# Performance work log

Hardware: AMD Instinct MI355X
Metric: run time of the kernel (lower is better)

The kernel has to match this reference:

```python
import jax, jax.numpy as jnp
import numpy as np

NUM_HEADS = 4
GROUPS = 32
EPS = 1e-5


def group_norm(x, gamma, beta):
    B, C, H, W = x.shape
    xg = x.reshape(B, GROUPS, C // GROUPS, H, W)
    mu = xg.mean(axis=(2, 3, 4), keepdims=True)
    var = xg.var(axis=(2, 3, 4), keepdims=True)
    xg = (xg - mu) * jax.lax.rsqrt(var + EPS)
    return xg.reshape(B, C, H, W) * gamma[None, :, None, None] + beta[None, :, None, None]


def setup_inputs() -> dict:
    key = jax.random.key(0)
    ks = jax.random.split(key, 6)
    B, C, H, W = 16, 256, 32, 32
    x = jax.random.normal(ks[0], (B, C, H, W), dtype=jnp.float32)
    gn_gamma = jnp.ones((C,), dtype=jnp.float32)
    gn_beta = jnp.zeros((C,), dtype=jnp.float32)
    # 1x1 convs are pure channel GEMMs; store weights as [out_ch, in_ch]
    qkv_w = jax.random.normal(ks[1], (3 * C, C), dtype=jnp.float32) * (C ** -0.5)
    qkv_b = jnp.zeros((3 * C,), dtype=jnp.float32)
    # NOTE: original zero-inits proj; we use small random weights so the
    # attention path is exercised/testable (see notes).
    proj_w = jax.random.normal(ks[2], (C, C), dtype=jnp.float32) * 0.02
    proj_b = jnp.zeros((C,), dtype=jnp.float32)
    return {"x": x, "gn_gamma": gn_gamma, "gn_beta": gn_beta,
            "qkv_w": qkv_w, "qkv_b": qkv_b, "proj_w": proj_w, "proj_b": proj_b}


def reference(x, gn_gamma, gn_beta, qkv_w, qkv_b, proj_w, proj_b):
    B, C, H, W = x.shape
    N = H * W
    d = C // NUM_HEADS
    h = group_norm(x, gn_gamma, gn_beta)
    hf = h.reshape(B, C, N)  # [B, C, N]
    qkv = jnp.einsum('oc,bcn->bon', qkv_w, hf) + qkv_b[None, :, None]
    qkv = qkv.reshape(B, NUM_HEADS, 3 * d, N)
    q, k, v = jnp.split(qkv, 3, axis=2)  # each [B, h, d, N]
    scale = d ** -0.5
    attn = jax.nn.softmax(jnp.einsum('bhdn,bhdm->bhnm', q, k) * scale, axis=-1)
    out = jnp.einsum('bhnm,bhdm->bhdn', attn, v).reshape(B, C, N)
    out = jnp.einsum('oc,bcn->bon', proj_w, out) + proj_b[None, :, None]
    return x + out.reshape(B, C, H, W)
```

## Files before the change

### kernel.cpp

```cpp
#include <hip/hip_runtime.h>

typedef short bf16x8_t __attribute__((ext_vector_type(8)));
typedef float f32x4_t __attribute__((ext_vector_type(4)));

__device__ __forceinline__ float bf2f(unsigned short h) {
  union { unsigned int u; float f; } v; v.u = ((unsigned int)h) << 16; return v.f;
}
__device__ __forceinline__ unsigned short f2bf(float f) {
  union { float f; unsigned int u; } v; v.f = f;
  unsigned int u = v.u + 0x7FFFu + ((v.u >> 16) & 1u);
  return (unsigned short)(u >> 16);
}
__device__ __forceinline__ unsigned int fbits(float f) {
  return __builtin_bit_cast(unsigned int, f);
}
__device__ __forceinline__ float exp2_hw(float x) {
  return __builtin_amdgcn_exp2f(x);
}
__device__ __forceinline__ unsigned int pack_trunc(float lo, float hi) {
  return __builtin_amdgcn_perm(fbits(hi), fbits(lo), 0x07060302u);
}
__device__ __forceinline__ void gload_lds16(const void* gsrc, void* ldst) {
  __builtin_amdgcn_global_load_lds(
      (const __attribute__((address_space(1))) unsigned int*)gsrc,
      (__attribute__((address_space(3))) unsigned int*)ldst, 16, 0, 0);
}

__device__ __align__(16) unsigned short g_hT[16 * 1024 * 256];
__device__ __align__(16) unsigned short g_qT[16 * 4 * 1024 * 64];
__device__ __align__(16) unsigned short g_kT[16 * 4 * 1024 * 64];
__device__ __align__(16) unsigned short g_vN[16 * 4 * 64 * 1024];
__device__ __align__(16) unsigned short g_wq[768 * 256];
__device__ __align__(16) unsigned short g_wp[256 * 256];

__global__ __launch_bounds__(256) void gn_kernel(
    const float* __restrict__ x, const float* __restrict__ gamma,
    const float* __restrict__ beta, const float* __restrict__ qkv_w,
    const float* __restrict__ proj_w) {
  const int b = blockIdx.x >> 5, g = blockIdx.x & 31;
  const int t = threadIdx.x;
  const float4* xg = (const float4*)(x + (size_t)(b * 256 + g * 8) * 1024);

  __shared__ __align__(16) unsigned short lds[8192];
  __shared__ float red[16];

  float vals[32];
  float s = 0.f, sq = 0.f;
#pragma unroll
  for (int p = 0; p < 4; ++p) {
    int idx = t + p * 256;
    float4 a = xg[2 * idx], c = xg[2 * idx + 1];
    float tmp[8] = {a.x, a.y, a.z, a.w, c.x, c.y, c.z, c.w};
#pragma unroll
    for (int j = 0; j < 8; ++j) {
      vals[p * 8 + j] = tmp[j];
      s += tmp[j]; sq += tmp[j] * tmp[j];
    }
  }

  {
    int widx = (blockIdx.x * 256 + t) * 2;
    const float* wsrc;
    unsigned short* wdst;
    if (widx < 196608) { wsrc = qkv_w + widx; wdst = g_wq + widx; }
    else { wsrc = proj_w + (widx - 196608); wdst = g_wp + (widx - 196608); }
    float2 wv = *(const float2*)wsrc;
    wdst[0] = f2bf(wv.x); wdst[1] = f2bf(wv.y);
  }

#pragma unroll
  for (int m = 32; m; m >>= 1) {
    s += __shfl_xor(s, m, 64);
    sq += __shfl_xor(sq, m, 64);
  }
  const int w = t >> 6;
  if ((t & 63) == 0) { red[w] = s; red[8 + w] = sq; }
  __syncthreads();
  s = red[0] + red[1] + red[2] + red[3];
  sq = red[8] + red[9] + red[10] + red[11];
  const float mu = s * (1.f / 8192.f);
  const float var = sq * (1.f / 8192.f) - mu * mu;
  const float rstd = rsqrtf(var + 1e-5f);

#pragma unroll
  for (int p = 0; p < 4; ++p) {
    int idx = t + p * 256;
    int c = idx >> 7;
    float ga = gamma[g * 8 + c] * rstd;
    float be = beta[g * 8 + c] - mu * ga;
    union { unsigned short u[8]; uint4 v; } pk;
#pragma unroll
    for (int j = 0; j < 8; ++j) pk.u[j] = f2bf(vals[p * 8 + j] * ga + be);
    ((uint4*)lds)[idx] = pk.v;
  }
  __syncthreads();

  unsigned short* dstbase = g_hT + (size_t)b * 1024 * 256 + g * 8;
#pragma unroll
  for (int p = 0; p < 4; ++p) {
    int n = t + p * 256;
    union { unsigned short u[8]; uint4 v; } pk;
#pragma unroll
    for (int c = 0; c < 8; ++c) pk.u[c] = lds[c * 1024 + n];
    *(uint4*)(dstbase + (size_t)n * 256) = pk.v;
  }
}

template <int MODE>
__global__ __launch_bounds__(256, 2) void gemm_ct(
    const float* __restrict__ bias, const float* __restrict__ xres,
    float* __restrict__ outp) {
  constexpr int OT = (MODE == 0) ? 96 : 64;
  constexpr int NT = (MODE == 0) ? 256 : 128;
  constexpr int OI = OT / 16;
  constexpr int NJ = NT / 64;
  constexpr int ASL = OT * 8;
  constexpr int BSL = NT * 8;

  const int n0 = blockIdx.x * NT;
  const int oty = blockIdx.y, o0 = oty * OT;
  const int b = blockIdx.z;
  const int t = threadIdx.x;
  const int w = t >> 6, lane = t & 63, quad = lane >> 4, l15 = lane & 15;

  __shared__ uint4 as[ASL];
  __shared__ uint4 bs[BSL];

  const uint4* Bv = (const uint4*)g_hT;
  const unsigned short* Wb = (MODE == 0) ? g_wq : g_wp;

  f32x4_t acc[OI][NJ];
#pragma unroll
  for (int i = 0; i < OI; ++i)
#pragma unroll
    for (int j = 0; j < NJ; ++j) acc[i][j] = (f32x4_t){0.f, 0.f, 0.f, 0.f};

  for (int kb = 0; kb < 4; ++kb) {
#pragma unroll
    for (int p = 0; p < ASL / 256; ++p) {
      int L = p * 256 + t;
      int row = L >> 3, kc = (L & 7) ^ (row & 7);
      gload_lds16(Wb + (size_t)(o0 + row) * 256 + kb * 64 + kc * 8,
                  &as[p * 256 + w * 64]);
    }
#pragma unroll
    for (int p = 0; p < BSL / 256; ++p) {
      int L = p * 256 + t;
      int row = L >> 3, kc = (L & 7) ^ (row & 7);
      gload_lds16(&Bv[(size_t)(b * 1024 + n0 + row) * 32 + kb * 8 + kc],
                  &bs[p * 256 + w * 64]);
    }
    __syncthreads();
#pragma unroll
    for (int kk = 0; kk < 2; ++kk) {
      int ch = kk * 4 + quad;
      const int sw = ch ^ (l15 & 7);
      bf16x8_t af[OI];
#pragma unroll
      for (int i = 0; i < OI; ++i)
        af[i] = __builtin_bit_cast(bf16x8_t, as[(i * 16 + l15) * 8 + sw]);
#pragma unroll
      for (int j = 0; j < NJ; ++j) {
        bf16x8_t bf = __builtin_bit_cast(
            bf16x8_t, bs[(w * (NT / 4) + j * 16 + l15) * 8 + sw]);
#pragma unroll
        for (int i = 0; i < OI; ++i)
          acc[i][j] = __builtin_amdgcn_mfma_f32_16x16x32_bf16(af[i], bf, acc[i][j], 0, 0, 0);
      }
    }
    __syncthreads();
  }

  float bi[OI][4];
#pragma unroll
  for (int i = 0; i < OI; ++i)
#pragma unroll
    for (int r = 0; r < 4; ++r) bi[i][r] = bias[o0 + i * 16 + quad * 4 + r];

  if (MODE == 0) {
#pragma unroll
    for (int i = 0; i < OI; ++i) {
      const int r0 = o0 + i * 16;
      const int head = r0 / 192;
      const int win = r0 - head * 192;
      const int type = win >> 6;
      const int d0 = (win & 63) + quad * 4;
      if (type < 2) {
        const float sc = (type == 0) ? 0.18033688f : 1.0f;
        unsigned short* dst = (type == 0 ? g_qT : g_kT) + (size_t)(b * 4 + head) * 65536;
#pragma unroll
        for (int j = 0; j < NJ; ++j) {
          int n = n0 + w * 64 + j * 16 + l15;
          ushort4 pk;
          pk.x = f2bf((acc[i][j][0] + bi[i][0]) * sc);
          pk.y = f2bf((acc[i][j][1] + bi[i][1]) * sc);
          pk.z = f2bf((acc[i][j][2] + bi[i][2]) * sc);
          pk.w = f2bf((acc[i][j][3] + bi[i][3]) * sc);
          *(ushort4*)(dst + (size_t)n * 64 + d0) = pk;
        }
      } else {
        unsigned short* dst = g_vN + (size_t)(b * 4 + head) * 65536;
#pragma unroll
        for (int j = 0; j < NJ; ++j) {
          int n = n0 + w * 64 + j * 16 + l15;
#pragma unroll
          for (int r = 0; r < 4; ++r)
            dst[(size_t)(d0 + r) * 1024 + n] = f2bf(acc[i][j][r] + bi[i][r]);
        }
      }
    }
  } else {
#pragma unroll
    for (int i = 0; i < OI; ++i)
#pragma unroll
      for (int r = 0; r < 4; ++r) {
        int c = o0 + i * 16 + quad * 4 + r;
        const float* xr = xres + (((size_t)b * 256 + c) << 10);
        float* op = outp + (((size_t)b * 256 + c) << 10);
#pragma unroll
        for (int j = 0; j < NJ; ++j) {
          int n = n0 + w * 32 + j * 16 + l15;
          op[n] = acc[i][j][r] + bi[i][r] + xr[n];
        }
      }
  }
}

__global__ __launch_bounds__(256) void attn_kernel() {
  const int bh = blockIdx.x;
  const int n0 = blockIdx.y * 128;
  const int t = threadIdx.x;
  const int w = t >> 6, lane = t & 63, quad = lane >> 4, l15 = lane & 15;
  const int b = bh >> 2, h = bh & 3;

  const uint4* qv = (const uint4*)(g_qT + (size_t)bh * 65536);
  const uint4* kv = (const uint4*)(g_kT + (size_t)bh * 65536);
  const uint4* vv = (const uint4*)(g_vN + (size_t)bh * 65536);

  __shared__ uint4 ks[2][512];
  __shared__ uint4 vs[2][512];
  __shared__ __align__(16) unsigned short Pt[2 * 4 * 16 * 72];

  uint4 qrA[2], qrB[2];
#pragma unroll
  for (int kk = 0; kk < 2; ++kk) {
    qrA[kk] = qv[(size_t)(n0 + w * 16 + l15) * 8 + kk * 4 + quad];
    qrB[kk] = qv[(size_t)(n0 + 64 + w * 16 + l15) * 8 + kk * 4 + quad];
  }

  const int rr0 = t >> 3, cc = t & 7, rr1 = rr0 + 32;
  uint4 kr0 = kv[rr0 * 8 + cc], kr1 = kv[rr1 * 8 + cc];
  uint4 vr0 = vv[rr0 * 128 + cc], vr1 = vv[rr1 * 128 + cc];

  f32x4_t OA[4], OB[4];
#pragma unroll
  for (int i = 0; i < 4; ++i) {
    OA[i] = (f32x4_t){0.f, 0.f, 0.f, 0.f};
    OB[i] = (f32x4_t){0.f, 0.f, 0.f, 0.f};
  }
  float rsumA = 0.f, rsumB = 0.f;

  unsigned short* PwA = Pt + w * 1152;
  unsigned short* PwB = Pt + 4608 + w * 1152;

#pragma unroll 1
  for (int mt = 0; mt < 16; ++mt) {
    uint4* kb = ks[mt & 1];
    uint4* vb = vs[mt & 1];
    kb[cc * 64 + (rr0 ^ cc)] = kr0; kb[cc * 64 + (rr1 ^ cc)] = kr1;
    vb[cc * 64 + (rr0 ^ cc)] = vr0; vb[cc * 64 + (rr1 ^ cc)] = vr1;
    __syncthreads();

    if (mt < 15) {
      int m1 = (mt + 1) * 64;
      kr0 = kv[(m1 + rr0) * 8 + cc]; kr1 = kv[(m1 + rr1) * 8 + cc];
      vr0 = vv[rr0 * 128 + (mt + 1) * 8 + cc]; vr1 = vv[rr1 * 128 + (mt + 1) * 8 + cc];
    }

    f32x4_t sA[4], sB[4];
#pragma unroll
    for (int i = 0; i < 4; ++i) {
      sA[i] = (f32x4_t){0.f, 0.f, 0.f, 0.f};
      sB[i] = (f32x4_t){0.f, 0.f, 0.f, 0.f};
    }
#pragma unroll
    for (int kk = 0; kk < 2; ++kk) {
      int ch = kk * 4 + quad;
      bf16x8_t bqA = __builtin_bit_cast(bf16x8_t, qrA[kk]);
      bf16x8_t bqB = __builtin_bit_cast(bf16x8_t, qrB[kk]);
#pragma unroll
      for (int ms = 0; ms < 4; ++ms) {
        bf16x8_t ak = __builtin_bit_cast(bf16x8_t, kb[ch * 64 + ((ms * 16 + l15) ^ ch)]);
        sA[ms] = __builtin_amdgcn_mfma_f32_16x16x32_bf16(ak, bqA, sA[ms], 0, 0, 0);
        sB[ms] = __builtin_amdgcn_mfma_f32_16x16x32_bf16(ak, bqB, sB[ms], 0, 0, 0);
      }
    }

#pragma unroll
    for (int ms = 0; ms < 4; ++ms) {
      float a0 = exp2_hw(sA[ms][0]), a1 = exp2_hw(sA[ms][1]);
      float a2 = exp2_hw(sA[ms][2]), a3 = exp2_hw(sA[ms][3]);
      float b0 = exp2_hw(sB[ms][0]), b1 = exp2_hw(sB[ms][1]);
      float b2 = exp2_hw(sB[ms][2]), b3 = exp2_hw(sB[ms][3]);
      rsumA += (a0 + a1) + (a2 + a3);
      rsumB += (b0 + b1) + (b2 + b3);
      uint2 pA, pB;
      pA.x = pack_trunc(a0, a1);
      pA.y = pack_trunc(a2, a3);
      pB.x = pack_trunc(b0, b1);
      pB.y = pack_trunc(b2, b3);
      *(uint2*)(PwA + l15 * 72 + ms * 16 + quad * 4) = pA;
      *(uint2*)(PwB + l15 * 72 + ms * 16 + quad * 4) = pB;
    }

#pragma unroll
    for (int km = 0; km < 2; ++km) {
      int ch = km * 4 + quad;
      bf16x8_t bpA = *(const bf16x8_t*)(PwA + l15 * 72 + km * 32 + quad * 8);
      bf16x8_t bpB = *(const bf16x8_t*)(PwB + l15 * 72 + km * 32 + quad * 8);
#pragma unroll
      for (int ds = 0; ds < 4; ++ds) {
        bf16x8_t av = __builtin_bit_cast(bf16x8_t, vb[ch * 64 + ((ds * 16 + l15) ^ ch)]);
        OA[ds] = __builtin_amdgcn_mfma_f32_16x16x32_bf16(av, bpA, OA[ds], 0, 0, 0);
        OB[ds] = __builtin_amdgcn_mfma_f32_16x16x32_bf16(av, bpB, OB[ds], 0, 0, 0);
      }
    }
  }

  rsumA += __shfl_xor(rsumA, 16, 64);
  rsumA += __shfl_xor(rsumA, 32, 64);
  rsumB += __shfl_xor(rsumB, 16, 64);
  rsumB += __shfl_xor(rsumB, 32, 64);
  const float invA = 1.f / rsumA, invB = 1.f / rsumB;

  unsigned short* dstA = g_hT + ((size_t)b * 1024 + n0 + w * 16 + l15) * 256 + h * 64;
  unsigned short* dstB = dstA + (size_t)64 * 256;
#pragma unroll
  for (int ds = 0; ds < 4; ++ds) {
    ushort4 pkA, pkB;
    pkA.x = f2bf(OA[ds][0] * invA); pkA.y = f2bf(OA[ds][1] * invA);
    pkA.z = f2bf(OA[ds][2] * invA); pkA.w = f2bf(OA[ds][3] * invA);
    pkB.x = f2bf(OB[ds][0] * invB); pkB.y = f2bf(OB[ds][1] * invB);
    pkB.z = f2bf(OB[ds][2] * invB); pkB.w = f2bf(OB[ds][3] * invB);
    *(ushort4*)(dstA + ds * 16 + quad * 4) = pkA;
    *(ushort4*)(dstB + ds * 16 + quad * 4) = pkB;
  }
}

extern "C" void kernel_launch(void* const* d_in, const int* in_sizes, int n_in,
                              void* d_out, int out_size, void* d_ws, size_t ws_size,
                              hipStream_t stream) {
  const float* x = (const float*)d_in[0];
  const float* gam = (const float*)d_in[1];
  const float* bet = (const float*)d_in[2];
  const float* qkv_w = (const float*)d_in[3];
  const float* qkv_b = (const float*)d_in[4];
  const float* pr_w = (const float*)d_in[5];
  const float* pr_b = (const float*)d_in[6];
  float* out = (float*)d_out;

  gn_kernel<<<512, 256, 0, stream>>>(x, gam, bet, qkv_w, pr_w);
  gemm_ct<0><<<dim3(4, 8, 16), 256, 0, stream>>>(qkv_b, nullptr, nullptr);
  attn_kernel<<<dim3(64, 8), 256, 0, stream>>>();
  gemm_ct<1><<<dim3(8, 4, 16), 256, 0, stream>>>(pr_b, x, out);
}
```

Before: 136.5 us.

## Halve attention query tile to double grid size, single-buffer K/V LDS

The attention kernel now handles 64 query rows per block instead of 128, doubling the grid from 512 to 1024 blocks, and adds a min-blocks-per-CU hint of 4 to launch bounds. K/V shared memory goes from double to single buffered, with an extra barrier at the end of each iteration. The aim is more occupancy and better CU coverage with less LDS and fewer registers per block. The cost is that each K/V tile is loaded twice as often in total, and each block now has two barriers per iteration with less MFMA work to hide latency.

```diff
diff --git a/kernel.cpp b/kernel.cpp
--- a/kernel.cpp
+++ b/kernel.cpp
@@ -226,9 +226,9 @@
   }
 }
 
-__global__ __launch_bounds__(256) void attn_kernel() {
+__global__ __launch_bounds__(256, 4) void attn_kernel() {
   const int bh = blockIdx.x;
-  const int n0 = blockIdx.y * 128;
+  const int n0 = blockIdx.y * 64;
   const int t = threadIdx.x;
   const int w = t >> 6, lane = t & 63, quad = lane >> 4, l15 = lane & 15;
   const int b = bh >> 2, h = bh & 3;
@@ -237,38 +237,30 @@
   const uint4* kv = (const uint4*)(g_kT + (size_t)bh * 65536);
   const uint4* vv = (const uint4*)(g_vN + (size_t)bh * 65536);
 
-  __shared__ uint4 ks[2][512];
-  __shared__ uint4 vs[2][512];
-  __shared__ __align__(16) unsigned short Pt[2 * 4 * 16 * 72];
-
-  uint4 qrA[2], qrB[2];
-#pragma unroll
-  for (int kk = 0; kk < 2; ++kk) {
-    qrA[kk] = qv[(size_t)(n0 + w * 16 + l15) * 8 + kk * 4 + quad];
-    qrB[kk] = qv[(size_t)(n0 + 64 + w * 16 + l15) * 8 + kk * 4 + quad];
-  }
+  __shared__ uint4 ks[512];
+  __shared__ uint4 vs[512];
+  __shared__ __align__(16) unsigned short Pt[4 * 16 * 72];
+
+  uint4 qr[2];
+#pragma unroll
+  for (int kk = 0; kk < 2; ++kk)
+    qr[kk] = qv[(size_t)(n0 + w * 16 + l15) * 8 + kk * 4 + quad];
 
   const int rr0 = t >> 3, cc = t & 7, rr1 = rr0 + 32;
   uint4 kr0 = kv[rr0 * 8 + cc], kr1 = kv[rr1 * 8 + cc];
   uint4 vr0 = vv[rr0 * 128 + cc], vr1 = vv[rr1 * 128 + cc];
 
-  f32x4_t OA[4], OB[4];
-#pragma unroll
-  for (int i = 0; i < 4; ++i) {
-    OA[i] = (f32x4_t){0.f, 0.f, 0.f, 0.f};
-    OB[i] = (f32x4_t){0.f, 0.f, 0.f, 0.f};
-  }
-  float rsumA = 0.f, rsumB = 0.f;
-
-  unsigned short* PwA = Pt + w * 1152;
-  unsigned short* PwB = Pt + 4608 + w * 1152;
+  f32x4_t OA[4];
+#pragma unroll
+  for (int i = 0; i < 4; ++i) OA[i] = (f32x4_t){0.f, 0.f, 0.f, 0.f};
+  float rsum = 0.f;
+
+  unsigned short* Pw = Pt + w * 1152;
 
 #pragma unroll 1
   for (int mt = 0; mt < 16; ++mt) {
-    uint4* kb = ks[mt & 1];
-    uint4* vb = vs[mt & 1];
-    kb[cc * 64 + (rr0 ^ cc)] = kr0; kb[cc * 64 + (rr1 ^ cc)] = kr1;
-    vb[cc * 64 + (rr0 ^ cc)] = vr0; vb[cc * 64 + (rr1 ^ cc)] = vr1;
+    ks[cc * 64 + (rr0 ^ cc)] = kr0; ks[cc * 64 + (rr1 ^ cc)] = kr1;
+    vs[cc * 64 + (rr0 ^ cc)] = vr0; vs[cc * 64 + (rr1 ^ cc)] = vr1;
     __syncthreads();
 
     if (mt < 15) {
@@ -277,22 +269,17 @@
       vr0 = vv[rr0 * 128 + (mt + 1) * 8 + cc]; vr1 = vv[rr1 * 128 + (mt + 1) * 8 + cc];
     }
 
-    f32x4_t sA[4], sB[4];
-#pragma unroll
-    for (int i = 0; i < 4; ++i) {
-      sA[i] = (f32x4_t){0.f, 0.f, 0.f, 0.f};
-      sB[i] = (f32x4_t){0.f, 0.f, 0.f, 0.f};
-    }
+    f32x4_t sA[4];
+#pragma unroll
+    for (int i = 0; i < 4; ++i) sA[i] = (f32x4_t){0.f, 0.f, 0.f, 0.f};
 #pragma unroll
     for (int kk = 0; kk < 2; ++kk) {
       int ch = kk * 4 + quad;
-      bf16x8_t bqA = __builtin_bit_cast(bf16x8_t, qrA[kk]);
-      bf16x8_t bqB = __builtin_bit_cast(bf16x8_t, qrB[kk]);
+      bf16x8_t bq = __builtin_bit_cast(bf16x8_t, qr[kk]);
 #pragma unroll
       for (int ms = 0; ms < 4; ++ms) {
-        bf16x8_t ak = __builtin_bit_cast(bf16x8_t, kb[ch * 64 + ((ms * 16 + l15) ^ ch)]);
-        sA[ms] = __builtin_amdgcn_mfma_f32_16x16x32_bf16(ak, bqA, sA[ms], 0, 0, 0);
-        sB[ms] = __builtin_amdgcn_mfma_f32_16x16x32_bf16(ak, bqB, sB[ms], 0, 0, 0);
+        bf16x8_t ak = __builtin_bit_cast(bf16x8_t, ks[ch * 64 + ((ms * 16 + l15) ^ ch)]);
+        sA[ms] = __builtin_amdgcn_mfma_f32_16x16x32_bf16(ak, bq, sA[ms], 0, 0, 0);
       }
     }
 
@@ -300,50 +287,37 @@
     for (int ms = 0; ms < 4; ++ms) {
       float a0 = exp2_hw(sA[ms][0]), a1 = exp2_hw(sA[ms][1]);
       float a2 = exp2_hw(sA[ms][2]), a3 = exp2_hw(sA[ms][3]);
-      float b0 = exp2_hw(sB[ms][0]), b1 = exp2_hw(sB[ms][1]);
-      float b2 = exp2_hw(sB[ms][2]), b3 = exp2_hw(sB[ms][3]);
-      rsumA += (a0 + a1) + (a2 + a3);
-      rsumB += (b0 + b1) + (b2 + b3);
-      uint2 pA, pB;
+      rsum += (a0 + a1) + (a2 + a3);
+      uint2 pA;
       pA.x = pack_trunc(a0, a1);
       pA.y = pack_trunc(a2, a3);
-      pB.x = pack_trunc(b0, b1);
-      pB.y = pack_trunc(b2, b3);
-      *(uint2*)(PwA + l15 * 72 + ms * 16 + quad * 4) = pA;
-      *(uint2*)(PwB + l15 * 72 + ms * 16 + quad * 4) = pB;
+      *(uint2*)(Pw + l15 * 72 + ms * 16 + quad * 4) = pA;
     }
 
 #pragma unroll
     for (int km = 0; km < 2; ++km) {
       int ch = km * 4 + quad;
-      bf16x8_t bpA = *(const bf16x8_t*)(PwA + l15 * 72 + km * 32 + quad * 8);
-      bf16x8_t bpB = *(const bf16x8_t*)(PwB + l15 * 72 + km * 32 + quad * 8);
+      bf16x8_t bp = *(const bf16x8_t*)(Pw + l15 * 72 + km * 32 + quad * 8);
 #pragma unroll
       for (int ds = 0; ds < 4; ++ds) {
-        bf16x8_t av = __builtin_bit_cast(bf16x8_t, vb[ch * 64 + ((ds * 16 + l15) ^ ch)]);
-        OA[ds] = __builtin_amdgcn_mfma_f32_16x16x32_bf16(av, bpA, OA[ds], 0, 0, 0);
-        OB[ds] = __builtin_amdgcn_mfma_f32_16x16x32_bf16(av, bpB, OB[ds], 0, 0, 0);
-      }
-    }
-  }
-
-  rsumA += __shfl_xor(rsumA, 16, 64);
-  rsumA += __shfl_xor(rsumA, 32, 64);
-  rsumB += __shfl_xor(rsumB, 16, 64);
-  rsumB += __shfl_xor(rsumB, 32, 64);
-  const float invA = 1.f / rsumA, invB = 1.f / rsumB;
+        bf16x8_t av = __builtin_bit_cast(bf16x8_t, vs[ch * 64 + ((ds * 16 + l15) ^ ch)]);
+        OA[ds] = __builtin_amdgcn_mfma_f32_16x16x32_bf16(av, bp, OA[ds], 0, 0, 0);
+      }
+    }
+    __syncthreads();
+  }
+
+  rsum += __shfl_xor(rsum, 16, 64);
+  rsum += __shfl_xor(rsum, 32, 64);
+  const float inv = 1.f / rsum;
 
   unsigned short* dstA = g_hT + ((size_t)b * 1024 + n0 + w * 16 + l15) * 256 + h * 64;
-  unsigned short* dstB = dstA + (size_t)64 * 256;
 #pragma unroll
   for (int ds = 0; ds < 4; ++ds) {
-    ushort4 pkA, pkB;
-    pkA.x = f2bf(OA[ds][0] * invA); pkA.y = f2bf(OA[ds][1] * invA);
-    pkA.z = f2bf(OA[ds][2] * invA); pkA.w = f2bf(OA[ds][3] * invA);
-    pkB.x = f2bf(OB[ds][0] * invB); pkB.y = f2bf(OB[ds][1] * invB);
-    pkB.z = f2bf(OB[ds][2] * invB); pkB.w = f2bf(OB[ds][3] * invB);
-    *(ushort4*)(dstA + ds * 16 + quad * 4) = pkA;
-    *(ushort4*)(dstB + ds * 16 + quad * 4) = pkB;
+    ushort4 pk;
+    pk.x = f2bf(OA[ds][0] * inv); pk.y = f2bf(OA[ds][1] * inv);
+    pk.z = f2bf(OA[ds][2] * inv); pk.w = f2bf(OA[ds][3] * inv);
+    *(ushort4*)(dstA + ds * 16 + quad * 4) = pk;
   }
 }
 
@@ -361,6 +335,6 @@
 
   gn_kernel<<<512, 256, 0, stream>>>(x, gam, bet, qkv_w, pr_w);
   gemm_ct<0><<<dim3(4, 8, 16), 256, 0, stream>>>(qkv_b, nullptr, nullptr);
-  attn_kernel<<<dim3(64, 8), 256, 0, stream>>>();
+  attn_kernel<<<dim3(64, 16), 256, 0, stream>>>();
   gemm_ct<1><<<dim3(8, 4, 16), 256, 0, stream>>>(pr_b, x, out);
 }
```

After: 140.9 us. 3.2% more time.
